# Optimization experiments

Hardware: AMD Instinct MI355X
Metric: run time of the kernel (lower is better)

Reference implementation:

```python
import jax, jax.numpy as jnp
import numpy as np

DIM = 512
HEADS = 8
EPS = 1e-12  # matches torch F.normalize default eps


def setup_inputs() -> dict:
    key = jax.random.key(0)
    k1, k2, k3, k4 = jax.random.split(key, 4)
    x = jax.random.normal(k1, (4, 2048, DIM), dtype=jnp.float32)
    # nn.Linear(dim, dim*3, bias=False): weight [3*dim, dim], y = x @ W.T
    w_qkv = jax.random.normal(k2, (3 * DIM, DIM), dtype=jnp.float32) * (1.0 / np.sqrt(DIM))
    w_out = jax.random.normal(k3, (DIM, DIM), dtype=jnp.float32) * (1.0 / np.sqrt(DIM))
    temperature = jnp.ones((HEADS, 1, 1), dtype=jnp.float32)
    return {"x": x, "w_qkv": w_qkv, "w_out": w_out, "temperature": temperature}


def _l2norm(t):
    # torch F.normalize(dim=-1): t / max(||t||, eps)
    n = jnp.sqrt(jnp.sum(t * t, axis=-1, keepdims=True))
    return t / jnp.maximum(n, EPS)


def reference(x, w_qkv, w_out, temperature):
    b, n, c = x.shape
    h = HEADS
    d = c // h
    qkv = x @ w_qkv.T  # [b, n, 3c]
    qkv = qkv.reshape(b, n, 3, h, d).transpose(2, 0, 3, 1, 4)  # [3, b, h, n, d]
    q, k, v = qkv[0], qkv[1], qkv[2]
    q = _l2norm(q)
    k = _l2norm(k)
    # cosine attention with learned per-head temperature
    attn = jnp.einsum("bhnd,bhmd->bhnm", q, k) * temperature  # temp broadcasts [h,1,1]
    attn = jax.nn.softmax(attn, axis=-1)
    out = jnp.einsum("bhnm,bhmd->bhnd", attn, v)  # [b, h, n, d]
    out = out.transpose(0, 2, 1, 3).reshape(b, n, c)
    return out @ w_out.T
```

## Files before the change

kernel.cpp:

```cpp
#include <hip/hip_runtime.h>
#include <hip/hip_bf16.h>

using bf16x8 = __attribute__((ext_vector_type(8))) short;
using f32x4  = __attribute__((ext_vector_type(4))) float;
using f32x16 = __attribute__((ext_vector_type(16))) float;
using u32x4  = __attribute__((ext_vector_type(4))) unsigned;

__device__ __forceinline__ short f2bf(float f) {
  union { float f; unsigned u; } v; v.f = f;
  unsigned r = (v.u + 0x7FFFu + ((v.u >> 16) & 1u)) >> 16;
  return (short)(unsigned short)r;
}

__device__ __forceinline__ unsigned cvtpk(float lo, float hi) {
  unsigned r;
  asm("v_cvt_pk_bf16_f32 %0, %1, %2" : "=v"(r) : "v"(lo), "v"(hi));
  return r;
}

__device__ __forceinline__ void plswap(unsigned &a, unsigned &b) {
  asm("v_permlane32_swap_b32 %0, %1" : "+v"(a), "+v"(b));
}

#define GLLDS(gp, lp) __builtin_amdgcn_global_load_lds(                        \
    (const __attribute__((address_space(1))) void*)(gp),                       \
    (__attribute__((address_space(3))) void*)(lp), 16, 0, 0)

__global__ __launch_bounds__(256)
void cvt_xw(const float* __restrict__ x, const float* __restrict__ wq,
            short* __restrict__ xb, short* __restrict__ wb)
{
  const int blk = blockIdx.x;
  const float* src;
  short* dst;
  int i;
  if (blk < 2048) { src = x;  dst = xb; i = blk * 256 + threadIdx.x; }
  else            { src = wq; dst = wb; i = (blk - 2048) * 256 + threadIdx.x; }
  float4 lo = *(const float4*)(src + (size_t)i * 8);
  float4 hi = *(const float4*)(src + (size_t)i * 8 + 4);
  uint4 r;
  r.x = cvtpk(lo.x, lo.y);
  r.y = cvtpk(lo.z, lo.w);
  r.z = cvtpk(hi.x, hi.y);
  r.w = cvtpk(hi.z, hi.w);
  *(uint4*)(dst + (size_t)i * 8) = r;
}

__global__ __launch_bounds__(256)
void cvt_f32_bf16(const float* __restrict__ in, short* __restrict__ out, int n8)
{
  int i = blockIdx.x * 256 + threadIdx.x;
  if (i >= n8) return;
  float4 lo = *(const float4*)(in + (size_t)i * 8);
  float4 hi = *(const float4*)(in + (size_t)i * 8 + 4);
  uint4 r;
  r.x = cvtpk(lo.x, lo.y);
  r.y = cvtpk(lo.z, lo.w);
  r.z = cvtpk(hi.x, hi.y);
  r.w = cvtpk(hi.z, hi.w);
  *(uint4*)(out + (size_t)i * 8) = r;
}

__global__ __launch_bounds__(256, 2)
void gemm_qkv(const short* __restrict__ A, const short* __restrict__ B,
              short* __restrict__ outQ, short* __restrict__ outK,
              short* __restrict__ outVt, const float* __restrict__ temp)
{
  __shared__ short As[128 * 32];
  __shared__ short Bs[128 * 32];
  const int Kd = 512;
  const int tid  = threadIdx.x;
  const int lane = tid & 63;
  const int w    = tid >> 6;
  const int wr   = w >> 1, wc = w & 1;
  const int fr   = lane & 15, fq = lane >> 4;
  const int bm = blockIdx.y, bn = blockIdx.x;
  const int rowA = bm * 128, rowB = bn * 128;

  const int lrow   = lane >> 2;
  const int lchunk = ((lane & 3) ^ ((lane >> 3) & 3)) * 8;
  const short* gA0 = A + (size_t)(rowA + w * 32 + lrow) * Kd + lchunk;
  const short* gB0 = B + (size_t)(rowB + w * 32 + lrow) * Kd + lchunk;
  char* lA0 = (char*)As + (w * 32) * 64;
  char* lB0 = (char*)Bs + (w * 32) * 64;
  const int rxor = ((fr >> 1) & 3) << 4;

  f32x4 acc[4][4];
  #pragma unroll
  for (int m = 0; m < 4; ++m)
    #pragma unroll
    for (int n = 0; n < 4; ++n) acc[m][n] = (f32x4){0.f, 0.f, 0.f, 0.f};

  for (int k0 = 0; k0 < Kd; k0 += 32) {
    GLLDS(gA0 + k0,            lA0);
    GLLDS(gA0 + k0 + 16 * Kd,  lA0 + 1024);
    GLLDS(gB0 + k0,            lB0);
    GLLDS(gB0 + k0 + 16 * Kd,  lB0 + 1024);
    __syncthreads();
    bf16x8 afr[4], bfr[4];
    #pragma unroll
    for (int m = 0; m < 4; ++m)
      afr[m] = *(const bf16x8*)((char*)As + (wr*64 + m*16 + fr) * 64 + ((fq*16) ^ rxor));
    #pragma unroll
    for (int n = 0; n < 4; ++n)
      bfr[n] = *(const bf16x8*)((char*)Bs + (wc*64 + n*16 + fr) * 64 + ((fq*16) ^ rxor));
    #pragma unroll
    for (int m = 0; m < 4; ++m)
      #pragma unroll
      for (int n = 0; n < 4; ++n)
        acc[m][n] = __builtin_amdgcn_mfma_f32_16x16x32_bf16(afr[m], bfr[n], acc[m][n], 0, 0, 0);
    __syncthreads();
  }

  const int gc0   = rowB + wc*64;
  const int slice = gc0 >> 6;
  const int t3    = slice >> 3;
  const int h     = slice & 7;
  if (t3 < 2) {
    float scl[4][4];
    const float tval = (t3 == 0) ? temp[h] * 1.44269504088896f : 1.0f;
    #pragma unroll
    for (int m = 0; m < 4; ++m) {
      #pragma unroll
      for (int r = 0; r < 4; ++r) {
        float ss = 0.f;
        #pragma unroll
        for (int n = 0; n < 4; ++n) ss += acc[m][n][r] * acc[m][n][r];
        #pragma unroll
        for (int off = 1; off < 16; off <<= 1) ss += __shfl_xor(ss, off);
        scl[m][r] = tval / fmaxf(sqrtf(ss), 1e-12f);
      }
    }
    short* dst = (t3 == 0) ? outQ : outK;
    #pragma unroll
    for (int m = 0; m < 4; ++m) {
      #pragma unroll
      for (int r = 0; r < 4; ++r) {
        int rg = rowA + wr*64 + m*16 + fq*4 + r;
        int b = rg >> 11, nn = rg & 2047;
        size_t rowoff = ((size_t)(b*8 + h) * 2048 + nn) * 64;
        #pragma unroll
        for (int n = 0; n < 4; ++n)
          dst[rowoff + n*16 + fr] = f2bf(acc[m][n][r] * scl[m][r]);
      }
    }
  } else {
    #pragma unroll
    for (int m = 0; m < 4; ++m) {
      #pragma unroll
      for (int r = 0; r < 4; ++r) {
        int rg = rowA + wr*64 + m*16 + fq*4 + r;
        int b = rg >> 11, nn = rg & 2047;
        #pragma unroll
        for (int n = 0; n < 4; ++n)
          outVt[((size_t)(b*8 + h) * 64 + n*16 + fr) * 2048 + nn] = f2bf(acc[m][n][r]);
      }
    }
  }
}

__global__ __launch_bounds__(256, 2)
void gemm_out(const short* __restrict__ A, const short* __restrict__ B,
              float* __restrict__ outC)
{
  __shared__ short As[128 * 32];
  __shared__ short Bs[64 * 32];
  const int Kd = 512, N = 512;
  const int tid  = threadIdx.x;
  const int lane = tid & 63;
  const int w    = tid >> 6;
  const int fr   = lane & 15, fq = lane >> 4;
  const int bm = blockIdx.y, bn = blockIdx.x;
  const int rowA = bm * 128, rowB = bn * 64;

  const int lrow   = lane >> 2;
  const int lchunk = ((lane & 3) ^ ((lane >> 3) & 3)) * 8;
  const short* gA0 = A + (size_t)(rowA + w * 32 + lrow) * Kd + lchunk;
  const short* gB0 = B + (size_t)(rowB + w * 16 + lrow) * Kd + lchunk;
  char* lA0 = (char*)As + (w * 32) * 64;
  char* lB0 = (char*)Bs + (w * 16) * 64;
  const int rxor = ((fr >> 1) & 3) << 4;

  f32x4 acc[2][4];
  #pragma unroll
  for (int m = 0; m < 2; ++m)
    #pragma unroll
    for (int n = 0; n < 4; ++n) acc[m][n] = (f32x4){0.f, 0.f, 0.f, 0.f};

  for (int k0 = 0; k0 < Kd; k0 += 32) {
    GLLDS(gA0 + k0,            lA0);
    GLLDS(gA0 + k0 + 16 * Kd,  lA0 + 1024);
    GLLDS(gB0 + k0,            lB0);
    __syncthreads();
    bf16x8 afr[2], bfr[4];
    #pragma unroll
    for (int m = 0; m < 2; ++m)
      afr[m] = *(const bf16x8*)((char*)As + (w*32 + m*16 + fr) * 64 + ((fq*16) ^ rxor));
    #pragma unroll
    for (int n = 0; n < 4; ++n)
      bfr[n] = *(const bf16x8*)((char*)Bs + (n*16 + fr) * 64 + ((fq*16) ^ rxor));
    #pragma unroll
    for (int m = 0; m < 2; ++m)
      #pragma unroll
      for (int n = 0; n < 4; ++n)
        acc[m][n] = __builtin_amdgcn_mfma_f32_16x16x32_bf16(afr[m], bfr[n], acc[m][n], 0, 0, 0);
    __syncthreads();
  }

  #pragma unroll
  for (int m = 0; m < 2; ++m) {
    int r0 = rowA + w*32 + m*16 + fq*4;
    #pragma unroll
    for (int n = 0; n < 4; ++n) {
      int c = rowB + n*16 + fr;
      #pragma unroll
      for (int r = 0; r < 4; ++r)
        outC[(size_t)(r0 + r) * N + c] = acc[m][n][r];
    }
  }
}

__global__ __launch_bounds__(256, 2)
void attn_fwd(const short* __restrict__ Q, const short* __restrict__ Kt,
              const short* __restrict__ Vt, short* __restrict__ AO,
              const float* __restrict__ temp)
{
  __shared__ short Kl[2][64 * 64];
  __shared__ short Vl[2][64 * 64];
  __shared__ float Ls[4][32];
  const int tid  = threadIdx.x;
  const int lane = tid & 63;
  const int w    = tid >> 6;
  const int l31  = lane & 31;
  const int hi   = lane >> 5;
  const int bh = blockIdx.x;
  const int qt = blockIdx.y;
  const int b = bh >> 3, h = bh & 7;
  const size_t base  = (size_t)bh * 2048 * 64;
  const size_t vbase = (size_t)bh * 64 * 2048;
  const int q0 = qt * 128 + w * 32;

  const short* kp = Kt + base;
  const short* vp = Vt + vbase;

  const int srow  = tid >> 3;
  const int scol8 = (tid & 7) * 8;
  const int scolB = (tid & 7) * 16;
  const int sxor  = (srow & 7) << 4;
  const int kswz  = (l31 & 7) << 4;

  bf16x8 stK[2], stV[2];
  #define LOAD_TILE(T)                                                              \
    do { int kt_ = (T) * 64;                                                        \
      stK[0] = *(const bf16x8*)(kp + (size_t)(kt_ + srow)      * 64 + scol8);       \
      stK[1] = *(const bf16x8*)(kp + (size_t)(kt_ + 32 + srow) * 64 + scol8);       \
      stV[0] = *(const bf16x8*)(vp + (size_t)srow        * 2048 + kt_ + scol8);     \
      stV[1] = *(const bf16x8*)(vp + (size_t)(32 + srow) * 2048 + kt_ + scol8);     \
    } while (0)
  #define WRITE_TILE(P_)                                                            \
    do {                                                                            \
      *(bf16x8*)((char*)Kl[P_] + (srow)      * 128 + (scolB ^ sxor)) = stK[0];      \
      *(bf16x8*)((char*)Kl[P_] + (32 + srow) * 128 + (scolB ^ sxor)) = stK[1];      \
      *(bf16x8*)((char*)Vl[P_] + (srow)      * 128 + (scolB ^ sxor)) = stV[0];      \
      *(bf16x8*)((char*)Vl[P_] + (32 + srow) * 128 + (scolB ^ sxor)) = stV[1];      \
    } while (0)

  bf16x8 bq[4];
  #pragma unroll
  for (int dj = 0; dj < 4; ++dj)
    bq[dj] = *(const bf16x8*)(Q + base + (size_t)(q0 + l31) * 64 + dj*16 + hi*8);

  const float Mh = fabsf(temp[h]) * 1.44269504088896f;
  f32x16 cinit;
  #pragma unroll
  for (int r = 0; r < 16; ++r) cinit[r] = -Mh;

  f32x16 o[2];
  #pragma unroll
  for (int td = 0; td < 2; ++td)
    #pragma unroll
    for (int r = 0; r < 16; ++r) o[td][r] = 0.f;
  float lp = 0.f;

  LOAD_TILE(0); WRITE_TILE(0);
  LOAD_TILE(1); WRITE_TILE(1);
  LOAD_TILE(2);
  __syncthreads();

  for (int t = 0; t < 32; ++t) {
    const int p = t & 1;
    const char* kl = (const char*)Kl[p];
    const char* vl = (const char*)Vl[p];

    f32x16 s[2];
    __builtin_amdgcn_s_setprio(1);
    #pragma unroll
    for (int tk = 0; tk < 2; ++tk) {
      f32x16 z = cinit;
      #pragma unroll
      for (int dj = 0; dj < 4; ++dj) {
        bf16x8 ak = *(const bf16x8*)(kl + (tk*32 + l31) * 128 + ((dj*32 + hi*16) ^ kswz));
        z = __builtin_amdgcn_mfma_f32_32x32x16_bf16(ak, bq[dj], z, 0, 0, 0);
      }
      s[tk] = z;
    }
    __builtin_amdgcn_s_setprio(0);
    #pragma unroll
    for (int tk = 0; tk < 2; ++tk)
      #pragma unroll
      for (int r = 0; r < 16; ++r) {
        float pv = __builtin_amdgcn_exp2f(s[tk][r]);
        s[tk][r] = pv;
        lp += pv;
      }
    bf16x8 pa[4];
    #pragma unroll
    for (int tk = 0; tk < 2; ++tk)
      #pragma unroll
      for (int j = 0; j < 2; ++j) {
        unsigned w0 = cvtpk(s[tk][8*j+0], s[tk][8*j+1]);
        unsigned w2 = cvtpk(s[tk][8*j+4], s[tk][8*j+5]);
        unsigned w1 = cvtpk(s[tk][8*j+2], s[tk][8*j+3]);
        unsigned w3 = cvtpk(s[tk][8*j+6], s[tk][8*j+7]);
        plswap(w0, w2);
        plswap(w1, w3);
        u32x4 pw = {w0, w1, w2, w3};
        pa[tk*2 + j] = __builtin_bit_cast(bf16x8, pw);
      }
    __builtin_amdgcn_s_setprio(1);
    #pragma unroll
    for (int td = 0; td < 2; ++td) {
      f32x16 acc = o[td];
      #pragma unroll
      for (int kj = 0; kj < 4; ++kj) {
        bf16x8 bv = *(const bf16x8*)(vl + (td*32 + l31) * 128 + ((kj*32 + hi*16) ^ kswz));
        acc = __builtin_amdgcn_mfma_f32_32x32x16_bf16(pa[kj], bv, acc, 0, 0, 0);
      }
      o[td] = acc;
    }
    __builtin_amdgcn_s_setprio(0);

    if (t < 31) {
      __syncthreads();
      if (t < 30) {
        WRITE_TILE(p);
        if (t < 29) LOAD_TILE(t + 3);
      }
    }
  }
  #undef LOAD_TILE
  #undef WRITE_TILE

  lp += __shfl_xor(lp, 32);
  if (hi == 0) Ls[w][l31] = 1.0f / lp;
  #pragma unroll
  for (int td = 0; td < 2; ++td)
    #pragma unroll
    for (int r = 0; r < 16; ++r) {
      int qr = (r & 3) + 8 * (r >> 2) + 4 * hi;
      float li = Ls[w][qr];
      int row = b * 2048 + q0 + qr;
      int col = h * 64 + td * 32 + l31;
      AO[(size_t)row * 512 + col] = f2bf(o[td][r] * li);
    }
}

extern "C" void kernel_launch(void* const* d_in, const int* in_sizes, int n_in,
                              void* d_out, int out_size, void* d_ws, size_t ws_size,
                              hipStream_t stream)
{
  const float* x     = (const float*)d_in[0];
  const float* w_qkv = (const float*)d_in[1];
  const float* w_out = (const float*)d_in[2];
  const float* temp  = (const float*)d_in[3];
  float* out = (float*)d_out;
  short* ws  = (short*)d_ws;

  const size_t NQ = (size_t)4 * 8 * 2048 * 64;
  short* Qb   = ws;
  short* Kb   = ws + NQ;
  short* Vtb  = ws + 2 * NQ;
  short* AO16 = ws + 3 * NQ;
  short* xb   = ws + 4 * NQ;
  short* wb   = AO16;
  short* wob  = xb;

  cvt_xw<<<dim3(2432), 256, 0, stream>>>(x, w_qkv, xb, wb);
  gemm_qkv<<<dim3(12, 64), 256, 0, stream>>>(xb, wb, Qb, Kb, Vtb, temp);
  cvt_f32_bf16<<<dim3(128), 256, 0, stream>>>(w_out, wob, 32768);
  attn_fwd<<<dim3(32, 16), 256, 0, stream>>>(Qb, Kb, Vtb, AO16, temp);
  gemm_out<<<dim3(8, 64), 256, 0, stream>>>(AO16, wob, out);
}
```

Measured before the change: 92.81 us.

## Software-pipeline attention loop so PV of previous tile overlaps current exp

Restructures the attention inner loop so the P·V MFMAs for tile t-1 are issued after the QK MFMAs for tile t. The exp/pack work for tile t can then overlap with matrix-core work. V fragments are read into registers early and carried across iterations, and the s_setprio hints are removed. This adds register pressure (two sets of V fragments plus packed P), which may lower occupancy or cause spills.

```diff
diff --git a/kernel.cpp b/kernel.cpp
--- a/kernel.cpp
+++ b/kernel.cpp
@@ -265,6 +265,68 @@
       *(bf16x8*)((char*)Vl[P_] + (32 + srow) * 128 + (scolB ^ sxor)) = stV[1];      \
     } while (0)
 
+  #define QK(SV, KL)                                                                \
+    do {                                                                            \
+      _Pragma("unroll")                                                             \
+      for (int tk = 0; tk < 2; ++tk) {                                              \
+        f32x16 z = cinit;                                                           \
+        _Pragma("unroll")                                                           \
+        for (int dj = 0; dj < 4; ++dj) {                                            \
+          bf16x8 ak = *(const bf16x8*)((KL) + (tk*32 + l31) * 128                   \
+                                            + ((dj*32 + hi*16) ^ kswz));            \
+          z = __builtin_amdgcn_mfma_f32_32x32x16_bf16(ak, bq[dj], z, 0, 0, 0);      \
+        }                                                                           \
+        SV[tk] = z;                                                                 \
+      }                                                                             \
+    } while (0)
+
+  #define READ_BV(BV, VL)                                                           \
+    do {                                                                            \
+      _Pragma("unroll")                                                             \
+      for (int td = 0; td < 2; ++td)                                                \
+        _Pragma("unroll")                                                           \
+        for (int kj = 0; kj < 4; ++kj)                                              \
+          BV[td][kj] = *(const bf16x8*)((VL) + (td*32 + l31) * 128                  \
+                                             + ((kj*32 + hi*16) ^ kswz));           \
+    } while (0)
+
+  #define EXP_PACK(SV)                                                              \
+    do {                                                                            \
+      _Pragma("unroll")                                                             \
+      for (int tk = 0; tk < 2; ++tk)                                                \
+        _Pragma("unroll")                                                           \
+        for (int r = 0; r < 16; ++r) {                                              \
+          float pv_ = __builtin_amdgcn_exp2f(SV[tk][r]);                            \
+          SV[tk][r] = pv_;                                                          \
+          lp += pv_;                                                                \
+        }                                                                           \
+      _Pragma("unroll")                                                             \
+      for (int tk = 0; tk < 2; ++tk)                                                \
+        _Pragma("unroll")                                                           \
+        for (int j = 0; j < 2; ++j) {                                               \
+          unsigned w0 = cvtpk(SV[tk][8*j+0], SV[tk][8*j+1]);                        \
+          unsigned w2 = cvtpk(SV[tk][8*j+4], SV[tk][8*j+5]);                        \
+          unsigned w1 = cvtpk(SV[tk][8*j+2], SV[tk][8*j+3]);                        \
+          unsigned w3 = cvtpk(SV[tk][8*j+6], SV[tk][8*j+7]);                        \
+          plswap(w0, w2); plswap(w1, w3);                                           \
+          u32x4 pw_ = {w0, w1, w2, w3};                                             \
+          paP[tk*2 + j] = __builtin_bit_cast(bf16x8, pw_);                          \
+        }                                                                           \
+    } while (0)
+
+  #define PV_PREV()                                                                 \
+    do {                                                                            \
+      _Pragma("unroll")                                                             \
+      for (int td = 0; td < 2; ++td) {                                              \
+        f32x16 acc_ = o[td];                                                        \
+        _Pragma("unroll")                                                           \
+        for (int kj = 0; kj < 4; ++kj)                                              \
+          acc_ = __builtin_amdgcn_mfma_f32_32x32x16_bf16(paP[kj], bvP[td][kj],      \
+                                                         acc_, 0, 0, 0);            \
+        o[td] = acc_;                                                               \
+      }                                                                             \
+    } while (0)
+
   bf16x8 bq[4];
   #pragma unroll
   for (int dj = 0; dj < 4; ++dj)
@@ -281,64 +343,42 @@
     #pragma unroll
     for (int r = 0; r < 16; ++r) o[td][r] = 0.f;
   float lp = 0.f;
+
+  bf16x8 paP[4];
+  bf16x8 bvP[2][4];
 
   LOAD_TILE(0); WRITE_TILE(0);
   LOAD_TILE(1); WRITE_TILE(1);
   LOAD_TILE(2);
   __syncthreads();
 
-  for (int t = 0; t < 32; ++t) {
+  {
+    const char* kl = (const char*)Kl[0];
+    const char* vl = (const char*)Vl[0];
+    f32x16 s[2];
+    QK(s, kl);
+    READ_BV(bvP, vl);
+    EXP_PACK(s);
+    __syncthreads();
+    WRITE_TILE(0);
+    LOAD_TILE(3);
+  }
+
+  for (int t = 1; t < 32; ++t) {
     const int p = t & 1;
     const char* kl = (const char*)Kl[p];
     const char* vl = (const char*)Vl[p];
 
     f32x16 s[2];
-    __builtin_amdgcn_s_setprio(1);
-    #pragma unroll
-    for (int tk = 0; tk < 2; ++tk) {
-      f32x16 z = cinit;
-      #pragma unroll
-      for (int dj = 0; dj < 4; ++dj) {
-        bf16x8 ak = *(const bf16x8*)(kl + (tk*32 + l31) * 128 + ((dj*32 + hi*16) ^ kswz));
-        z = __builtin_amdgcn_mfma_f32_32x32x16_bf16(ak, bq[dj], z, 0, 0, 0);
-      }
-      s[tk] = z;
-    }
-    __builtin_amdgcn_s_setprio(0);
-    #pragma unroll
-    for (int tk = 0; tk < 2; ++tk)
-      #pragma unroll
-      for (int r = 0; r < 16; ++r) {
-        float pv = __builtin_amdgcn_exp2f(s[tk][r]);
-        s[tk][r] = pv;
-        lp += pv;
-      }
-    bf16x8 pa[4];
-    #pragma unroll
-    for (int tk = 0; tk < 2; ++tk)
-      #pragma unroll
-      for (int j = 0; j < 2; ++j) {
-        unsigned w0 = cvtpk(s[tk][8*j+0], s[tk][8*j+1]);
-        unsigned w2 = cvtpk(s[tk][8*j+4], s[tk][8*j+5]);
-        unsigned w1 = cvtpk(s[tk][8*j+2], s[tk][8*j+3]);
-        unsigned w3 = cvtpk(s[tk][8*j+6], s[tk][8*j+7]);
-        plswap(w0, w2);
-        plswap(w1, w3);
-        u32x4 pw = {w0, w1, w2, w3};
-        pa[tk*2 + j] = __builtin_bit_cast(bf16x8, pw);
-      }
-    __builtin_amdgcn_s_setprio(1);
-    #pragma unroll
-    for (int td = 0; td < 2; ++td) {
-      f32x16 acc = o[td];
-      #pragma unroll
-      for (int kj = 0; kj < 4; ++kj) {
-        bf16x8 bv = *(const bf16x8*)(vl + (td*32 + l31) * 128 + ((kj*32 + hi*16) ^ kswz));
-        acc = __builtin_amdgcn_mfma_f32_32x32x16_bf16(pa[kj], bv, acc, 0, 0, 0);
-      }
-      o[td] = acc;
-    }
-    __builtin_amdgcn_s_setprio(0);
+    QK(s, kl);
+    bf16x8 bvC[2][4];
+    READ_BV(bvC, vl);
+    PV_PREV();
+    EXP_PACK(s);
+    #pragma unroll
+    for (int td = 0; td < 2; ++td)
+      #pragma unroll
+      for (int kj = 0; kj < 4; ++kj) bvP[td][kj] = bvC[td][kj];
 
     if (t < 31) {
       __syncthreads();
@@ -348,8 +388,14 @@
       }
     }
   }
+  PV_PREV();
+
   #undef LOAD_TILE
   #undef WRITE_TILE
+  #undef QK
+  #undef READ_BV
+  #undef EXP_PACK
+  #undef PV_PREV
 
   lp += __shfl_xor(lp, 32);
   if (hi == 0) Ls[w][l31] = 1.0f / lp;
```

Result: no change. 93.00 us (+0.2%).

## Store K/V in MFMA fragment order and stream directly to registers in attention

Applied to the files above, without the earlier changes.

The QKV GEMM epilogue now writes K and V in a pre-swizzled fragment layout, so each lane's MFMA operand is one contiguous 16-byte global load. The attention kernel drops LDS staging and barriers entirely, loading K/V fragments straight into registers with a software-pipelined schedule that interleaves QK, PV and exp across two 32-query groups per wave. Each block now covers 256 queries, which halves the grid and reuses each K/V fetch across more queries. In exchange, register pressure rises (launch bounds lowered to one block per SM), the grid has only 256 blocks, and every wave reloads K/V from global/L2 instead of sharing them through LDS.

```diff
diff --git a/kernel.cpp b/kernel.cpp
--- a/kernel.cpp
+++ b/kernel.cpp
@@ -63,8 +63,8 @@
 
 __global__ __launch_bounds__(256, 2)
 void gemm_qkv(const short* __restrict__ A, const short* __restrict__ B,
-              short* __restrict__ outQ, short* __restrict__ outK,
-              short* __restrict__ outVt, const float* __restrict__ temp)
+              short* __restrict__ outQ, short* __restrict__ outKF,
+              short* __restrict__ outVF, const float* __restrict__ temp)
 {
   __shared__ short As[128 * 32];
   __shared__ short Bs[128 * 32];
@@ -131,29 +131,51 @@
         scl[m][r] = tval / fmaxf(sqrtf(ss), 1e-12f);
       }
     }
-    short* dst = (t3 == 0) ? outQ : outK;
-    #pragma unroll
-    for (int m = 0; m < 4; ++m) {
-      #pragma unroll
-      for (int r = 0; r < 4; ++r) {
-        int rg = rowA + wr*64 + m*16 + fq*4 + r;
-        int b = rg >> 11, nn = rg & 2047;
-        size_t rowoff = ((size_t)(b*8 + h) * 2048 + nn) * 64;
+    if (t3 == 0) {
+      #pragma unroll
+      for (int m = 0; m < 4; ++m) {
         #pragma unroll
-        for (int n = 0; n < 4; ++n)
-          dst[rowoff + n*16 + fr] = f2bf(acc[m][n][r] * scl[m][r]);
+        for (int r = 0; r < 4; ++r) {
+          int rg = rowA + wr*64 + m*16 + fq*4 + r;
+          int b = rg >> 11, nn = rg & 2047;
+          size_t rowoff = ((size_t)(b*8 + h) * 2048 + nn) * 64;
+          #pragma unroll
+          for (int n = 0; n < 4; ++n)
+            outQ[rowoff + n*16 + fr] = f2bf(acc[m][n][r] * scl[m][r]);
+        }
+      }
+    } else {
+      const int hi8 = fr >> 3, e = fr & 7;
+      #pragma unroll
+      for (int m = 0; m < 4; ++m) {
+        #pragma unroll
+        for (int r = 0; r < 4; ++r) {
+          int rg = rowA + wr*64 + m*16 + fq*4 + r;
+          int b = rg >> 11, tokn = rg & 2047;
+          int kt = tokn >> 6, tk = (tokn >> 5) & 1, l31k = tokn & 31;
+          size_t fb = (size_t)(b*8 + h) * 131072;
+          #pragma unroll
+          for (int n = 0; n < 4; ++n)
+            outKF[fb + (size_t)((kt*8 + tk*4 + n) * 64 + hi8*32 + l31k) * 8 + e] =
+                f2bf(acc[m][n][r] * scl[m][r]);
+        }
       }
     }
   } else {
+    const int b   = rowA >> 11;
+    const int kt  = ((rowA & 2047) >> 6) + wr;
+    const int hiv = (fq >> 1) & 1;
+    const int e0  = (fq & 1) * 4;
+    size_t fb = (size_t)(b*8 + h) * 131072;
     #pragma unroll
     for (int m = 0; m < 4; ++m) {
       #pragma unroll
-      for (int r = 0; r < 4; ++r) {
-        int rg = rowA + wr*64 + m*16 + fq*4 + r;
-        int b = rg >> 11, nn = rg & 2047;
-        #pragma unroll
-        for (int n = 0; n < 4; ++n)
-          outVt[((size_t)(b*8 + h) * 64 + n*16 + fr) * 2048 + nn] = f2bf(acc[m][n][r]);
+      for (int n = 0; n < 4; ++n) {
+        unsigned lo = cvtpk(acc[m][n][0], acc[m][n][1]);
+        unsigned hi = cvtpk(acc[m][n][2], acc[m][n][3]);
+        size_t off = fb + (size_t)((kt*8 + (n >> 1)*4 + m) * 64
+                                   + hiv*32 + (n & 1)*16 + fr) * 8 + e0;
+        *(uint2*)(outVF + off) = make_uint2(lo, hi);
       }
     }
   }
@@ -220,14 +242,12 @@
   }
 }
 
-__global__ __launch_bounds__(256, 2)
-void attn_fwd(const short* __restrict__ Q, const short* __restrict__ Kt,
-              const short* __restrict__ Vt, short* __restrict__ AO,
+__global__ __launch_bounds__(256, 1)
+void attn_fwd(const short* __restrict__ Q, const short* __restrict__ KF,
+              const short* __restrict__ VF, short* __restrict__ AO,
               const float* __restrict__ temp)
 {
-  __shared__ short Kl[2][64 * 64];
-  __shared__ short Vl[2][64 * 64];
-  __shared__ float Ls[4][32];
+  __shared__ float Ls[4][64];
   const int tid  = threadIdx.x;
   const int lane = tid & 63;
   const int w    = tid >> 6;
@@ -237,132 +257,139 @@
   const int qt = blockIdx.y;
   const int b = bh >> 3, h = bh & 7;
   const size_t base  = (size_t)bh * 2048 * 64;
-  const size_t vbase = (size_t)bh * 64 * 2048;
-  const int q0 = qt * 128 + w * 32;
-
-  const short* kp = Kt + base;
-  const short* vp = Vt + vbase;
-
-  const int srow  = tid >> 3;
-  const int scol8 = (tid & 7) * 8;
-  const int scolB = (tid & 7) * 16;
-  const int sxor  = (srow & 7) << 4;
-  const int kswz  = (l31 & 7) << 4;
-
-  bf16x8 stK[2], stV[2];
-  #define LOAD_TILE(T)                                                              \
-    do { int kt_ = (T) * 64;                                                        \
-      stK[0] = *(const bf16x8*)(kp + (size_t)(kt_ + srow)      * 64 + scol8);       \
-      stK[1] = *(const bf16x8*)(kp + (size_t)(kt_ + 32 + srow) * 64 + scol8);       \
-      stV[0] = *(const bf16x8*)(vp + (size_t)srow        * 2048 + kt_ + scol8);     \
-      stV[1] = *(const bf16x8*)(vp + (size_t)(32 + srow) * 2048 + kt_ + scol8);     \
-    } while (0)
-  #define WRITE_TILE(P_)                                                            \
-    do {                                                                            \
-      *(bf16x8*)((char*)Kl[P_] + (srow)      * 128 + (scolB ^ sxor)) = stK[0];      \
-      *(bf16x8*)((char*)Kl[P_] + (32 + srow) * 128 + (scolB ^ sxor)) = stK[1];      \
-      *(bf16x8*)((char*)Vl[P_] + (srow)      * 128 + (scolB ^ sxor)) = stV[0];      \
-      *(bf16x8*)((char*)Vl[P_] + (32 + srow) * 128 + (scolB ^ sxor)) = stV[1];      \
-    } while (0)
-
-  bf16x8 bq[4];
-  #pragma unroll
-  for (int dj = 0; dj < 4; ++dj)
-    bq[dj] = *(const bf16x8*)(Q + base + (size_t)(q0 + l31) * 64 + dj*16 + hi*8);
+  const size_t fbase = (size_t)bh * 131072;
+  const int q0 = qt * 256 + w * 64;
+
+  const short* kf = KF + fbase + (size_t)lane * 8;
+  const short* vf = VF + fbase + (size_t)lane * 8;
+
+  bf16x8 bq[2][4];
+  #pragma unroll
+  for (int qg = 0; qg < 2; ++qg)
+    #pragma unroll
+    for (int dj = 0; dj < 4; ++dj)
+      bq[qg][dj] = *(const bf16x8*)(Q + base + (size_t)(q0 + qg*32 + l31) * 64 + dj*16 + hi*8);
 
   const float Mh = fabsf(temp[h]) * 1.44269504088896f;
   f32x16 cinit;
   #pragma unroll
   for (int r = 0; r < 16; ++r) cinit[r] = -Mh;
 
-  f32x16 o[2];
-  #pragma unroll
-  for (int td = 0; td < 2; ++td)
-    #pragma unroll
-    for (int r = 0; r < 16; ++r) o[td][r] = 0.f;
-  float lp = 0.f;
-
-  LOAD_TILE(0); WRITE_TILE(0);
-  LOAD_TILE(1); WRITE_TILE(1);
-  LOAD_TILE(2);
-  __syncthreads();
-
-  for (int t = 0; t < 32; ++t) {
-    const int p = t & 1;
-    const char* kl = (const char*)Kl[p];
-    const char* vl = (const char*)Vl[p];
-
+  f32x16 o[2][2];
+  #pragma unroll
+  for (int qg = 0; qg < 2; ++qg)
+    #pragma unroll
+    for (int td = 0; td < 2; ++td)
+      #pragma unroll
+      for (int r = 0; r < 16; ++r) o[qg][td][r] = 0.f;
+  float lp0 = 0.f, lp1 = 0.f;
+
+  bf16x8 ak[8], bv[8], paP[2][4];
+
+  #define LOADK(T)                                                             \
+    do { _Pragma("unroll")                                                     \
+      for (int j_ = 0; j_ < 8; ++j_)                                           \
+        ak[j_] = *(const bf16x8*)(kf + ((size_t)(T)*8 + j_) * 512);            \
+    } while (0)
+  #define LOADV(T)                                                             \
+    do { _Pragma("unroll")                                                     \
+      for (int j_ = 0; j_ < 8; ++j_)                                           \
+        bv[j_] = *(const bf16x8*)(vf + ((size_t)(T)*8 + j_) * 512);            \
+    } while (0)
+  #define QKG(QG, SS)                                                          \
+    do { _Pragma("unroll")                                                     \
+      for (int tk_ = 0; tk_ < 2; ++tk_) {                                      \
+        f32x16 z_ = cinit;                                                     \
+        _Pragma("unroll")                                                      \
+        for (int dj_ = 0; dj_ < 4; ++dj_)                                      \
+          z_ = __builtin_amdgcn_mfma_f32_32x32x16_bf16(ak[tk_*4 + dj_],        \
+                                                       bq[QG][dj_], z_, 0,0,0);\
+        SS[tk_] = z_;                                                          \
+      }                                                                        \
+    } while (0)
+  #define EXPPACK(QG, SS, LP)                                                  \
+    do { _Pragma("unroll")                                                     \
+      for (int tk_ = 0; tk_ < 2; ++tk_)                                        \
+        _Pragma("unroll")                                                      \
+        for (int r_ = 0; r_ < 16; ++r_) {                                      \
+          float p_ = __builtin_amdgcn_exp2f(SS[tk_][r_]);                      \
+          SS[tk_][r_] = p_;                                                    \
+          LP += p_;                                                            \
+        }                                                                      \
+      _Pragma("unroll")                                                        \
+      for (int tk_ = 0; tk_ < 2; ++tk_)                                        \
+        _Pragma("unroll")                                                      \
+        for (int j_ = 0; j_ < 2; ++j_) {                                       \
+          unsigned w0 = cvtpk(SS[tk_][8*j_+0], SS[tk_][8*j_+1]);               \
+          unsigned w2 = cvtpk(SS[tk_][8*j_+4], SS[tk_][8*j_+5]);               \
+          unsigned w1 = cvtpk(SS[tk_][8*j_+2], SS[tk_][8*j_+3]);               \
+          unsigned w3 = cvtpk(SS[tk_][8*j_+6], SS[tk_][8*j_+7]);               \
+          plswap(w0, w2); plswap(w1, w3);                                      \
+          u32x4 pw_ = {w0, w1, w2, w3};                                        \
+          paP[QG][tk_*2 + j_] = __builtin_bit_cast(bf16x8, pw_);               \
+        }                                                                      \
+    } while (0)
+  #define PVG(QG)                                                              \
+    do { _Pragma("unroll")                                                     \
+      for (int td_ = 0; td_ < 2; ++td_) {                                      \
+        f32x16 a_ = o[QG][td_];                                                \
+        _Pragma("unroll")                                                      \
+        for (int kj_ = 0; kj_ < 4; ++kj_)                                      \
+          a_ = __builtin_amdgcn_mfma_f32_32x32x16_bf16(paP[QG][kj_],           \
+                                                       bv[td_*4 + kj_], a_,    \
+                                                       0, 0, 0);               \
+        o[QG][td_] = a_;                                                       \
+      }                                                                        \
+    } while (0)
+
+  {
+    LOADK(0);
     f32x16 s[2];
-    __builtin_amdgcn_s_setprio(1);
-    #pragma unroll
-    for (int tk = 0; tk < 2; ++tk) {
-      f32x16 z = cinit;
-      #pragma unroll
-      for (int dj = 0; dj < 4; ++dj) {
-        bf16x8 ak = *(const bf16x8*)(kl + (tk*32 + l31) * 128 + ((dj*32 + hi*16) ^ kswz));
-        z = __builtin_amdgcn_mfma_f32_32x32x16_bf16(ak, bq[dj], z, 0, 0, 0);
+    QKG(0, s);
+    EXPPACK(0, s, lp0);
+    QKG(1, s);
+    LOADV(0);
+    EXPPACK(1, s, lp1);
+  }
+
+  for (int t = 1; t < 32; ++t) {
+    LOADK(t);
+    f32x16 s[2];
+    QKG(0, s);
+    PVG(0);
+    EXPPACK(0, s, lp0);
+    QKG(1, s);
+    PVG(1);
+    LOADV(t);
+    EXPPACK(1, s, lp1);
+  }
+  PVG(0);
+  PVG(1);
+
+  #undef LOADK
+  #undef LOADV
+  #undef QKG
+  #undef EXPPACK
+  #undef PVG
+
+  lp0 += __shfl_xor(lp0, 32);
+  lp1 += __shfl_xor(lp1, 32);
+  if (hi == 0) {
+    Ls[w][l31]      = 1.0f / lp0;
+    Ls[w][32 + l31] = 1.0f / lp1;
+  }
+  #pragma unroll
+  for (int qg = 0; qg < 2; ++qg)
+    #pragma unroll
+    for (int td = 0; td < 2; ++td)
+      #pragma unroll
+      for (int r = 0; r < 16; ++r) {
+        int qr = (r & 3) + 8 * (r >> 2) + 4 * hi;
+        float li = Ls[w][qg*32 + qr];
+        int row = b * 2048 + q0 + qg*32 + qr;
+        int col = h * 64 + td * 32 + l31;
+        AO[(size_t)row * 512 + col] = f2bf(o[qg][td][r] * li);
       }
-      s[tk] = z;
-    }
-    __builtin_amdgcn_s_setprio(0);
-    #pragma unroll
-    for (int tk = 0; tk < 2; ++tk)
-      #pragma unroll
-      for (int r = 0; r < 16; ++r) {
-        float pv = __builtin_amdgcn_exp2f(s[tk][r]);
-        s[tk][r] = pv;
-        lp += pv;
-      }
-    bf16x8 pa[4];
-    #pragma unroll
-    for (int tk = 0; tk < 2; ++tk)
-      #pragma unroll
-      for (int j = 0; j < 2; ++j) {
-        unsigned w0 = cvtpk(s[tk][8*j+0], s[tk][8*j+1]);
-        unsigned w2 = cvtpk(s[tk][8*j+4], s[tk][8*j+5]);
-        unsigned w1 = cvtpk(s[tk][8*j+2], s[tk][8*j+3]);
-        unsigned w3 = cvtpk(s[tk][8*j+6], s[tk][8*j+7]);
-        plswap(w0, w2);
-        plswap(w1, w3);
-        u32x4 pw = {w0, w1, w2, w3};
-        pa[tk*2 + j] = __builtin_bit_cast(bf16x8, pw);
-      }
-    __builtin_amdgcn_s_setprio(1);
-    #pragma unroll
-    for (int td = 0; td < 2; ++td) {
-      f32x16 acc = o[td];
-      #pragma unroll
-      for (int kj = 0; kj < 4; ++kj) {
-        bf16x8 bv = *(const bf16x8*)(vl + (td*32 + l31) * 128 + ((kj*32 + hi*16) ^ kswz));
-        acc = __builtin_amdgcn_mfma_f32_32x32x16_bf16(pa[kj], bv, acc, 0, 0, 0);
-      }
-      o[td] = acc;
-    }
-    __builtin_amdgcn_s_setprio(0);
-
-    if (t < 31) {
-      __syncthreads();
-      if (t < 30) {
-        WRITE_TILE(p);
-        if (t < 29) LOAD_TILE(t + 3);
-      }
-    }
-  }
-  #undef LOAD_TILE
-  #undef WRITE_TILE
-
-  lp += __shfl_xor(lp, 32);
-  if (hi == 0) Ls[w][l31] = 1.0f / lp;
-  #pragma unroll
-  for (int td = 0; td < 2; ++td)
-    #pragma unroll
-    for (int r = 0; r < 16; ++r) {
-      int qr = (r & 3) + 8 * (r >> 2) + 4 * hi;
-      float li = Ls[w][qr];
-      int row = b * 2048 + q0 + qr;
-      int col = h * 64 + td * 32 + l31;
-      AO[(size_t)row * 512 + col] = f2bf(o[td][r] * li);
-    }
 }
 
 extern "C" void kernel_launch(void* const* d_in, const int* in_sizes, int n_in,
@@ -378,16 +405,16 @@
 
   const size_t NQ = (size_t)4 * 8 * 2048 * 64;
   short* Qb   = ws;
-  short* Kb   = ws + NQ;
-  short* Vtb  = ws + 2 * NQ;
+  short* KFb  = ws + NQ;
+  short* VFb  = ws + 2 * NQ;
   short* AO16 = ws + 3 * NQ;
   short* xb   = ws + 4 * NQ;
   short* wb   = AO16;
   short* wob  = xb;
 
   cvt_xw<<<dim3(2432), 256, 0, stream>>>(x, w_qkv, xb, wb);
-  gemm_qkv<<<dim3(12, 64), 256, 0, stream>>>(xb, wb, Qb, Kb, Vtb, temp);
+  gemm_qkv<<<dim3(12, 64), 256, 0, stream>>>(xb, wb, Qb, KFb, VFb, temp);
   cvt_f32_bf16<<<dim3(128), 256, 0, stream>>>(w_out, wob, 32768);
-  attn_fwd<<<dim3(32, 16), 256, 0, stream>>>(Qb, Kb, Vtb, AO16, temp);
+  attn_fwd<<<dim3(32, 8), 256, 0, stream>>>(Qb, KFb, VFb, AO16, temp);
   gemm_out<<<dim3(8, 64), 256, 0, stream>>>(AO16, wob, out);
 }
```

Measured after the change: 99.31 us. 7.0% more time.
